# Performance work log

Hardware: AMD Instinct MI355X
Metric: run time of the kernel (lower is better)

Reference implementation:

```python
import jax, jax.numpy as jnp
import numpy as np

B, N, C = 16, 1024, 256
NH, DH = 8, 32          # dense attention heads
NHD, P = 8, 4           # deformable heads / sampling points
Hs = Ws = 32            # value spatial grid (N == Hs*Ws)
HID = 1024              # mlp hidden = 4*C


def setup_inputs() -> dict:
    key = jax.random.key(0)
    ks = jax.random.split(key, 16)
    rn = lambda i, shape, s=1.0: jax.random.normal(ks[i], shape, jnp.float32) * s
    return {
        "x": rn(0, (B, N, C)),
        "ref": jax.random.uniform(ks[1], (B, N, 2), jnp.float32),
        "value": rn(2, (B, N, C)),
        "ln1_w": jnp.ones((C,), jnp.float32), "ln1_b": jnp.zeros((C,), jnp.float32),
        "ln2_w": jnp.ones((C,), jnp.float32), "ln2_b": jnp.zeros((C,), jnp.float32),
        "ln3_w": jnp.ones((C,), jnp.float32), "ln3_b": jnp.zeros((C,), jnp.float32),
        "qkv_w": rn(3, (3 * C, C), 0.05),
        "proj_w": rn(4, (C, C), 0.05), "proj_b": jnp.zeros((C,), jnp.float32),
        "off_w": rn(5, (NHD * P * 2, C), 0.01), "off_b": rn(6, (NHD * P * 2,), 0.5),
        "aw_w": rn(7, (NHD * P, C), 0.01), "aw_b": jnp.zeros((NHD * P,), jnp.float32),
        "vproj_w": rn(8, (C, C), 0.05), "vproj_b": jnp.zeros((C,), jnp.float32),
        "oproj_w": rn(9, (C, C), 0.05), "oproj_b": jnp.zeros((C,), jnp.float32),
        "fc1_w": rn(10, (HID, C), 0.05), "fc1_b": jnp.zeros((HID,), jnp.float32),
        "fc2_w": rn(11, (C, HID), 0.05), "fc2_b": jnp.zeros((C,), jnp.float32),
    }


def _ln(x, w, b):
    m = x.mean(-1, keepdims=True)
    v = ((x - m) ** 2).mean(-1, keepdims=True)
    return (x - m) * jax.lax.rsqrt(v + 1e-5) * w + b


def _attn(x, qkv_w, proj_w, proj_b):
    qkv = (x @ qkv_w.T).reshape(B, N, 3, NH, DH)
    q, k, v = qkv[:, :, 0], qkv[:, :, 1], qkv[:, :, 2]
    a = jnp.einsum('bqhd,bkhd->bhqk', q, k) * (DH ** -0.5)
    a = jax.nn.softmax(a, axis=-1)
    o = jnp.einsum('bhqk,bkhd->bqhd', a, v).reshape(B, N, C)
    return o @ proj_w.T + proj_b


def _deform(q, ref, value, off_w, off_b, aw_w, aw_b, vproj_w, vproj_b, oproj_w, oproj_b):
    # single-level MS deformable attention (Deformable-DETR style)
    v = (value @ vproj_w.T + vproj_b).reshape(B, Hs * Ws, NHD, DH)
    off = (q @ off_w.T + off_b).reshape(B, N, NHD, P, 2)
    aw = jax.nn.softmax((q @ aw_w.T + aw_b).reshape(B, N, NHD, P), axis=-1)
    norm = jnp.array([Ws, Hs], jnp.float32)
    loc = ref[:, :, None, None, :] + off / norm  # [B,N,NHD,P,2] normalized coords
    gx = loc[..., 0] * Ws - 0.5
    gy = loc[..., 1] * Hs - 0.5
    x0 = jnp.floor(gx); y0 = jnp.floor(gy)
    lx = gx - x0; ly = gy - y0
    x0i = x0.astype(jnp.int32); y0i = y0.astype(jnp.int32)
    b_idx = jnp.arange(B)[:, None, None, None]
    h_idx = jnp.arange(NHD)[None, None, :, None]

    def gather(xi, yi):
        valid = ((xi >= 0) & (xi < Ws) & (yi >= 0) & (yi < Hs)).astype(jnp.float32)
        idx = jnp.clip(yi, 0, Hs - 1) * Ws + jnp.clip(xi, 0, Ws - 1)
        return v[b_idx, idx, h_idx] * valid[..., None]  # [B,N,NHD,P,DH]

    s = (gather(x0i, y0i) * ((1 - lx) * (1 - ly))[..., None]
         + gather(x0i + 1, y0i) * (lx * (1 - ly))[..., None]
         + gather(x0i, y0i + 1) * ((1 - lx) * ly)[..., None]
         + gather(x0i + 1, y0i + 1) * (lx * ly)[..., None])
    out = (s * aw[..., None]).sum(axis=3).reshape(B, N, C)
    return out @ oproj_w.T + oproj_b


def reference(x, ref, value, ln1_w, ln1_b, ln2_w, ln2_b, ln3_w, ln3_b,
              qkv_w, proj_w, proj_b, off_w, off_b, aw_w, aw_b,
              vproj_w, vproj_b, oproj_w, oproj_b, fc1_w, fc1_b, fc2_w, fc2_b):
    x = x + _attn(_ln(x, ln1_w, ln1_b), qkv_w, proj_w, proj_b)
    x = x + _deform(_ln(x, ln2_w, ln2_b), ref, value,
                    off_w, off_b, aw_w, aw_b, vproj_w, vproj_b, oproj_w, oproj_b)
    h = jax.nn.gelu(_ln(x, ln3_w, ln3_b) @ fc1_w.T + fc1_b, approximate=False) @ fc2_w.T + fc2_b
    return x + h
```

## Files before the change

kernel.cpp:

```cpp
#include <hip/hip_runtime.h>
#include <hip/hip_bf16.h>

#define Bq   16
#define Nq   1024
#define Cq   256
#define NHq  8
#define DHq  32
#define HIDq 1024
#define BNq  (Bq * Nq)

typedef float f32x4 __attribute__((ext_vector_type(4)));
typedef short bf16x8 __attribute__((ext_vector_type(8)));
typedef unsigned int u32x4 __attribute__((ext_vector_type(4)));
typedef unsigned short ushort_t;

__device__ __forceinline__ unsigned int f2bf(float f) {
    unsigned int u = __builtin_bit_cast(unsigned int, f);
    u = (u + 0x7fffu + ((u >> 16) & 1u)) >> 16;
    return u & 0xffffu;
}
__device__ __forceinline__ unsigned int packbf2(float a, float b) {
    unsigned int ua = __builtin_bit_cast(unsigned int, a) + 0x8000u;
    unsigned int ub = __builtin_bit_cast(unsigned int, b) + 0x8000u;
    return __builtin_amdgcn_perm(ub, ua, 0x07060302);
}
__device__ __forceinline__ unsigned int cvtpk_bf16(float lo, float hi) {
    unsigned int r;
    asm("v_cvt_pk_bf16_f32 %0, %1, %2" : "=v"(r) : "v"(lo), "v"(hi));
    return r;
}
__device__ __forceinline__ float gelu_t(float x) {
    float y = x * (0.7978845608028654f + 0.035677408136300125f * x * x);
    float e = __builtin_amdgcn_exp2f(y * 2.8853900817779268f);
    return x - x / (1.f + e);
}

typedef __attribute__((address_space(1))) const unsigned int* gas_u32;
typedef __attribute__((address_space(3))) unsigned int* las_u32;
__device__ __forceinline__ void gload16(const void* g, void* l) {
    __builtin_amdgcn_global_load_lds((gas_u32)g, (las_u32)l, 16, 0, 0);
}

struct CastSeg { const float* src; ushort_t* dst; int nblk; int n; };
struct CastArgs { CastSeg s[9]; };

__global__ __launch_bounds__(256) void castm(CastArgs a) {
    int bid = blockIdx.x;
    int seg = 0, acc = 0;
    for (seg = 0; seg < 9; seg++) {
        if (bid < acc + a.s[seg].nblk) break;
        acc += a.s[seg].nblk;
    }
    const CastSeg sg = a.s[seg];
    int i = (bid - acc) * 1024 + threadIdx.x * 4;
    if (i < sg.n) {
        float4 v = *(const float4*)(sg.src + i);
        uint2 u;
        u.x = packbf2(v.x, v.y);
        u.y = packbf2(v.z, v.w);
        *(uint2*)(sg.dst + i) = u;
    }
}

__global__ __launch_bounds__(256) void ln_kernel(const float* __restrict__ X,
                                                 const float* __restrict__ w,
                                                 const float* __restrict__ b,
                                                 ushort_t* __restrict__ Y) {
    int wave = threadIdx.x >> 6, lane = threadIdx.x & 63;
    int t = blockIdx.x * 4 + wave;
    float4 v = *(const float4*)(X + (size_t)t * Cq + lane * 4);
    float s = v.x + v.y + v.z + v.w;
#pragma unroll
    for (int d = 1; d < 64; d <<= 1) s += __shfl_xor(s, d);
    float mean = s * (1.f / 256.f);
    float4 dv = {v.x - mean, v.y - mean, v.z - mean, v.w - mean};
    float q = dv.x * dv.x + dv.y * dv.y + dv.z * dv.z + dv.w * dv.w;
#pragma unroll
    for (int d = 1; d < 64; d <<= 1) q += __shfl_xor(q, d);
    float rs = rsqrtf(q * (1.f / 256.f) + 1e-5f);
    float4 wv = *(const float4*)(w + lane * 4);
    float4 bv = *(const float4*)(b + lane * 4);
    uint2 u;
    u.x = packbf2(dv.x * rs * wv.x + bv.x, dv.y * rs * wv.y + bv.y);
    u.y = packbf2(dv.z * rs * wv.z + bv.z, dv.w * rs * wv.w + bv.w);
    *(uint2*)(Y + (size_t)t * Cq + lane * 4) = u;
}

template <int OMODE, bool GELU_, bool RESID, int KT>
__global__ __launch_bounds__(256) void mgemm(const ushort_t* __restrict__ A,
                                             const ushort_t* __restrict__ W,
                                             const float* __restrict__ bias,
                                             const float* __restrict__ R,
                                             void* __restrict__ OutP,
                                             int M, int Nn) {
    __shared__ __align__(16) ushort_t Al[2][8192];
    __shared__ __align__(16) ushort_t Bl[2][4096];
    int m0 = blockIdx.x * 128, n0 = blockIdx.y * 64;
    int tid = threadIdx.x;
    int w = tid >> 6, lane = tid & 63;
    int l15 = lane & 15, quad = lane >> 4;

    f32x4 acc[2][4];
#pragma unroll
    for (int i = 0; i < 2; i++)
#pragma unroll
        for (int j = 0; j < 4; j++) acc[i][j] = (f32x4){0.f, 0.f, 0.f, 0.f};

    const ushort_t* gA0 = A + (size_t)(m0 + lane) * KT + w * 8;
    const ushort_t* gA1 = gA0 + (size_t)64 * KT;
    const ushort_t* gB0 = W + (size_t)(n0 + lane) * KT + w * 8;

    auto STAGE = [&](int buf, int t) {
        const int k0 = t * 64;
        gload16(gA0 + k0,      &Al[buf][w * 1024]);
        gload16(gA1 + k0,      &Al[buf][w * 1024 + 512]);
        gload16(gA0 + k0 + 32, &Al[buf][(w + 4) * 1024]);
        gload16(gA1 + k0 + 32, &Al[buf][(w + 4) * 1024 + 512]);
        gload16(gB0 + k0,      &Bl[buf][w * 512]);
        gload16(gB0 + k0 + 32, &Bl[buf][(w + 4) * 512]);
    };

    constexpr int NT = KT / 64;
    STAGE(0, 0);
    STAGE(1, 1);
    asm volatile("s_waitcnt vmcnt(6)" ::: "memory");
    __builtin_amdgcn_s_barrier();

#pragma unroll
    for (int t = 0; t < NT; t++) {
        const int cur = t & 1;
        bf16x8 aF[2][2], bF[2][4];
#pragma unroll
        for (int ks = 0; ks < 2; ks++) {
#pragma unroll
            for (int i = 0; i < 2; i++)
                aF[ks][i] = *(const bf16x8*)&Al[cur][(ks * 4 + quad) * 1024 + (w * 32 + i * 16 + l15) * 8];
#pragma unroll
            for (int j = 0; j < 4; j++)
                bF[ks][j] = *(const bf16x8*)&Bl[cur][(ks * 4 + quad) * 512 + (j * 16 + l15) * 8];
        }
        asm volatile("s_waitcnt lgkmcnt(0)" ::: "memory");
        __builtin_amdgcn_sched_barrier(0);
        __builtin_amdgcn_s_barrier();
        if (t + 2 < NT) STAGE(cur, t + 2);

        __builtin_amdgcn_s_setprio(1);
#pragma unroll
        for (int ks = 0; ks < 2; ks++)
#pragma unroll
            for (int i = 0; i < 2; i++)
#pragma unroll
                for (int j = 0; j < 4; j++)
                    acc[i][j] = __builtin_amdgcn_mfma_f32_16x16x32_bf16(bF[ks][j], aF[ks][i], acc[i][j], 0, 0, 0);
        __builtin_amdgcn_s_setprio(0);

        if (t + 2 < NT) {
            asm volatile("s_waitcnt vmcnt(6)" ::: "memory");
        } else if (t + 1 < NT) {
            asm volatile("s_waitcnt vmcnt(0)" ::: "memory");
        }
        if (t + 1 < NT) __builtin_amdgcn_s_barrier();
    }

#pragma unroll
    for (int i = 0; i < 2; i++) {
        int mg = m0 + w * 32 + i * 16 + l15;
#pragma unroll
        for (int j = 0; j < 4; j++) {
            int ng = n0 + j * 16 + quad * 4;
            f32x4 rv = acc[i][j];
            if constexpr (OMODE == 1) {
                int which = ng >> 8;
                int h = (ng >> 5) & 7;
                int d = ng & 31;
                int bb = mg >> 10, nn = mg & 1023;
                ushort_t* qb = (ushort_t*)OutP;
                if (which == 2) {
                    size_t dst = 2 * (size_t)BNq * Cq +
                                 ((size_t)(bb * 8 + h) * 32 + d) * 1024 + nn;
#pragma unroll
                    for (int r = 0; r < 4; r++)
                        qb[dst + (size_t)r * 1024] = (ushort_t)f2bf(rv[r]);
                } else {
                    if (which == 0) {
                        const float sc = 0.17677669529663687f * 1.4426950408889634f;
                        rv[0] *= sc; rv[1] *= sc; rv[2] *= sc; rv[3] *= sc;
                    }
                    size_t dst = (size_t)which * ((size_t)BNq * Cq) +
                                 ((size_t)(bb * 8 + h) * 1024 + nn) * 32 + d;
                    uint2 pk;
                    pk.x = packbf2(rv[0], rv[1]);
                    pk.y = packbf2(rv[2], rv[3]);
                    *(uint2*)(qb + dst) = pk;
                }
            } else if constexpr (OMODE == 3) {
                if (ng >= 96) continue;
                if (ng < 64) {
                    float4 bv = *(const float4*)(bias + ng);
                    rv[0] += bv.x; rv[1] += bv.y; rv[2] += bv.z; rv[3] += bv.w;
                    *(float4*)((float*)OutP + (size_t)mg * 64 + ng) =
                        make_float4(rv[0], rv[1], rv[2], rv[3]);
                } else {
                    float4 bv = *(const float4*)(R + (ng - 64));
                    rv[0] += bv.x; rv[1] += bv.y; rv[2] += bv.z; rv[3] += bv.w;
                    *(float4*)((float*)OutP + (size_t)BNq * 64 + (size_t)mg * 32 + (ng - 64)) =
                        make_float4(rv[0], rv[1], rv[2], rv[3]);
                }
            } else {
                if (bias) {
                    float4 bv = *(const float4*)(bias + ng);
                    rv[0] += bv.x; rv[1] += bv.y; rv[2] += bv.z; rv[3] += bv.w;
                }
                if (GELU_) {
#pragma unroll
                    for (int r = 0; r < 4; r++) rv[r] = gelu_t(rv[r]);
                }
                if constexpr (OMODE == 2) {
                    uint2 pk;
                    pk.x = packbf2(rv[0], rv[1]);
                    pk.y = packbf2(rv[2], rv[3]);
                    *(uint2*)((ushort_t*)OutP + (size_t)mg * Nn + ng) = pk;
                } else {
                    if (RESID) {
                        float4 rr = *(const float4*)(R + (size_t)mg * Nn + ng);
                        rv[0] += rr.x; rv[1] += rr.y; rv[2] += rr.z; rv[3] += rr.w;
                    }
                    *(float4*)((float*)OutP + (size_t)mg * Nn + ng) =
                        make_float4(rv[0], rv[1], rv[2], rv[3]);
                }
            }
        }
    }
}

__global__ __launch_bounds__(256) void mlp_fused(const float* __restrict__ X,
                                                 const ushort_t* __restrict__ W1,
                                                 const float* __restrict__ b1,
                                                 const ushort_t* __restrict__ W2,
                                                 const float* __restrict__ b2,
                                                 const float* __restrict__ lnw,
                                                 const float* __restrict__ lnb,
                                                 float* __restrict__ out) {
    __shared__ __align__(16) ushort_t W1l[16384];
    __shared__ __align__(16) ushort_t W2l[8192];
    __shared__ __align__(16) ushort_t Hl[4096];
    __shared__ __align__(16) float b1l[1024];
    __shared__ __align__(16) float lnwl[256];
    __shared__ __align__(16) float lnbl[256];
    int bid = blockIdx.x;
    int m0 = (bid >> 1) * 64;
    int nh = bid & 1;
    int tid = threadIdx.x;
    int w = tid >> 6, lane = tid & 63;
    int l15 = lane & 15, quad = lane >> 4;

    auto SW1 = [&](int ch) {
        const ushort_t* g = W1 + (size_t)(ch * 64 + lane) * 256 + w * 8;
#pragma unroll
        for (int j = 0; j < 8; j++)
            gload16(g + j * 32, &W1l[(w + 4 * j) * 512]);
    };
    auto SW2 = [&](int ch) {
#pragma unroll
        for (int jj = 0; jj < 4; jj++) {
            const int kc2 = (jj & 1) * 4 + w;
            const int rj = jj >> 1;
            const ushort_t* g = W2 + (size_t)(nh * 128 + rj * 64 + lane) * 1024 +
                                ch * 64 + (kc2 & 3) * 8 + (kc2 >> 2) * 32;
            gload16(g, &W2l[kc2 * 1024 + rj * 512]);
        }
    };

    f32x4 acc2[4][2];
#pragma unroll
    for (int i = 0; i < 4; i++)
#pragma unroll
        for (int j = 0; j < 2; j++) acc2[i][j] = (f32x4){0.f, 0.f, 0.f, 0.f};

    SW1(0);
    SW2(0);
    gload16(b1 + w * 256 + lane * 4, &b1l[w * 256]);
    if (w == 0) gload16(lnw + lane * 4, &lnwl[0]);
    if (w == 1) gload16(lnb + lane * 4, &lnbl[0]);

    float4 xv[16];
    {
        const float* gx = X + (size_t)(m0 + w * 16 + l15) * 256 + quad * 8;
#pragma unroll
        for (int ks = 0; ks < 8; ks++) {
            xv[2 * ks]     = *(const float4*)(gx + ks * 32);
            xv[2 * ks + 1] = *(const float4*)(gx + ks * 32 + 4);
        }
    }
    asm volatile("s_waitcnt vmcnt(0)" ::: "memory");
    __builtin_amdgcn_s_barrier();

    float s = 0.f;
#pragma unroll
    for (int i = 0; i < 16; i++) s += xv[i].x + xv[i].y + xv[i].z + xv[i].w;
    s += __shfl_xor(s, 16);
    s += __shfl_xor(s, 32);
    float mean = s * (1.f / 256.f);
    float q = 0.f;
#pragma unroll
    for (int i = 0; i < 16; i++) {
        float a0 = xv[i].x - mean, a1 = xv[i].y - mean;
        float a2 = xv[i].z - mean, a3 = xv[i].w - mean;
        q += a0 * a0 + a1 * a1 + a2 * a2 + a3 * a3;
    }
    q += __shfl_xor(q, 16);
    q += __shfl_xor(q, 32);
    float rs = rsqrtf(q * (1.f / 256.f) + 1e-5f);

    bf16x8 aF[8];
#pragma unroll
    for (int ks = 0; ks < 8; ks++) {
        const int kb = ks * 32 + quad * 8;
        float y0 = (xv[2 * ks].x - mean) * rs * lnwl[kb + 0] + lnbl[kb + 0];
        float y1 = (xv[2 * ks].y - mean) * rs * lnwl[kb + 1] + lnbl[kb + 1];
        float y2 = (xv[2 * ks].z - mean) * rs * lnwl[kb + 2] + lnbl[kb + 2];
        float y3 = (xv[2 * ks].w - mean) * rs * lnwl[kb + 3] + lnbl[kb + 3];
        float y4 = (xv[2 * ks + 1].x - mean) * rs * lnwl[kb + 4] + lnbl[kb + 4];
        float y5 = (xv[2 * ks + 1].y - mean) * rs * lnwl[kb + 5] + lnbl[kb + 5];
        float y6 = (xv[2 * ks + 1].z - mean) * rs * lnwl[kb + 6] + lnbl[kb + 6];
        float y7 = (xv[2 * ks + 1].w - mean) * rs * lnwl[kb + 7] + lnbl[kb + 7];
        u32x4 up;
        up.x = cvtpk_bf16(y0, y1);
        up.y = cvtpk_bf16(y2, y3);
        up.z = cvtpk_bf16(y4, y5);
        up.w = cvtpk_bf16(y6, y7);
        aF[ks] = __builtin_bit_cast(bf16x8, up);
    }

    for (int ch = 0; ch < 16; ch++) {
        f32x4 acc1[4];
#pragma unroll
        for (int j = 0; j < 4; j++) acc1[j] = (f32x4){0.f, 0.f, 0.f, 0.f};
#pragma unroll
        for (int ks = 0; ks < 8; ks++) {
            bf16x8 bF[4];
#pragma unroll
            for (int j = 0; j < 4; j++)
                bF[j] = *(const bf16x8*)&W1l[(ks * 4 + quad) * 512 + (j * 16 + l15) * 8];
#pragma unroll
            for (int j = 0; j < 4; j++)
                acc1[j] = __builtin_amdgcn_mfma_f32_16x16x32_bf16(bF[j], aF[ks], acc1[j], 0, 0, 0);
        }
#pragma unroll
        for (int j = 0; j < 4; j++) {
            float4 b1v = *(const float4*)&b1l[ch * 64 + j * 16 + quad * 4];
            f32x4 rv = acc1[j];
            rv[0] = gelu_t(rv[0] + b1v.x);
            rv[1] = gelu_t(rv[1] + b1v.y);
            rv[2] = gelu_t(rv[2] + b1v.z);
            rv[3] = gelu_t(rv[3] + b1v.w);
            int h = j * 16 + quad * 4;
            uint2 pk;
            pk.x = cvtpk_bf16(rv[0], rv[1]);
            pk.y = cvtpk_bf16(rv[2], rv[3]);
            *(uint2*)&Hl[((h >> 3) * 64 + (w * 16 + l15)) * 8 + (h & 7)] = pk;
        }
        asm volatile("s_waitcnt lgkmcnt(0)" ::: "memory");
        __builtin_amdgcn_sched_barrier(0);
        __builtin_amdgcn_s_barrier();
        if (ch + 1 < 16) {
            SW1(ch + 1);
            asm volatile("s_waitcnt vmcnt(8)" ::: "memory");
        } else {
            asm volatile("s_waitcnt vmcnt(0)" ::: "memory");
        }
        __builtin_amdgcn_s_barrier();

        __builtin_amdgcn_s_setprio(1);
#pragma unroll
        for (int ks2 = 0; ks2 < 2; ks2++) {
            bf16x8 a2[4], b2f[2];
#pragma unroll
            for (int i = 0; i < 4; i++)
                a2[i] = *(const bf16x8*)&Hl[(ks2 * 4 + quad) * 512 + (i * 16 + l15) * 8];
#pragma unroll
            for (int j = 0; j < 2; j++)
                b2f[j] = *(const bf16x8*)&W2l[(ks2 * 4 + quad) * 1024 + (w * 32 + j * 16 + l15) * 8];
#pragma unroll
            for (int i = 0; i < 4; i++)
#pragma unroll
                for (int j = 0; j < 2; j++)
                    acc2[i][j] = __builtin_amdgcn_mfma_f32_16x16x32_bf16(b2f[j], a2[i], acc2[i][j], 0, 0, 0);
        }
        __builtin_amdgcn_s_setprio(0);
        asm volatile("s_waitcnt lgkmcnt(0)" ::: "memory");
        __builtin_amdgcn_sched_barrier(0);
        __builtin_amdgcn_s_barrier();
        if (ch + 1 < 16) {
            SW2(ch + 1);
            asm volatile("s_waitcnt vmcnt(4)" ::: "memory");
            __builtin_amdgcn_s_barrier();
        }
    }

#pragma unroll
    for (int i = 0; i < 4; i++) {
        int mg = m0 + i * 16 + l15;
#pragma unroll
        for (int j = 0; j < 2; j++) {
            int ng = nh * 128 + w * 32 + j * 16 + quad * 4;
            f32x4 rv = acc2[i][j];
            float4 bv = *(const float4*)(b2 + ng);
            float4 rr = *(const float4*)(X + (size_t)mg * 256 + ng);
            rv[0] += bv.x + rr.x; rv[1] += bv.y + rr.y;
            rv[2] += bv.z + rr.z; rv[3] += bv.w + rr.w;
            *(float4*)(out + (size_t)mg * 256 + ng) =
                make_float4(rv[0], rv[1], rv[2], rv[3]);
        }
    }
}

__global__ __launch_bounds__(256, 4) void attn_mfma(const ushort_t* __restrict__ Qb,
                                                    const ushort_t* __restrict__ Kb,
                                                    const ushort_t* __restrict__ Vtg,
                                                    ushort_t* __restrict__ o) {
    int bh = blockIdx.x;
    int b = bh >> 3, h = bh & 7;
    int q0 = blockIdx.y * 128;
    int tid = threadIdx.x;
    int wave = tid >> 6, lane = tid & 63;
    int l15 = lane & 15, quad = lane >> 4;

    __shared__ __align__(16) ushort_t Ks[2][64][40];
    __shared__ __align__(16) ushort_t Vs[2][32][88];
    __shared__ __align__(16) ushort_t Ps[4][32][72];

    const size_t hb = (size_t)bh * 32768;

    bf16x8 qfrag[2];
#pragma unroll
    for (int g = 0; g < 2; g++)
        qfrag[g] = *(const bf16x8*)(Qb + hb + (size_t)(q0 + wave * 32 + g * 16 + l15) * 32 + quad * 8);

    f32x4 oa[2][2];
#pragma unroll
    for (int g = 0; g < 2; g++)
#pragma unroll
        for (int t = 0; t < 2; t++) oa[g][t] = (f32x4){0.f, 0.f, 0.f, 0.f};
    f32x4 ls[2];
    ls[0] = (f32x4){0.f, 0.f, 0.f, 0.f};
    ls[1] = (f32x4){0.f, 0.f, 0.f, 0.f};

    bf16x8 ones;
#pragma unroll
    for (int i = 0; i < 8; i++) ones[i] = (short)0x3F80;

    int krow = tid >> 2, kch = tid & 3;
    int vrow = tid >> 3, vch = tid & 7;
    const ushort_t* kgp = Kb + hb + (size_t)krow * 32 + kch * 8;
    const ushort_t* vgp = Vtg + hb + (size_t)vrow * 1024 + vch * 8;

    bf16x8 kreg = *(const bf16x8*)kgp;
    bf16x8 vreg = *(const bf16x8*)vgp;

#pragma unroll 2
    for (int kt = 0; kt < 16; kt++) {
        const int cur = kt & 1;
        *(bf16x8*)&Ks[cur][krow][kch * 8] = kreg;
        *(bf16x8*)&Vs[cur][vrow][vch * 8] = vreg;
        __syncthreads();
        if (kt < 15) {
            kreg = *(const bf16x8*)(kgp + (kt + 1) * 2048);
            vreg = *(const bf16x8*)(vgp + (kt + 1) * 64);
        }

        bf16x8 kf[4];
#pragma unroll
        for (int kg = 0; kg < 4; kg++)
            kf[kg] = *(const bf16x8*)&Ks[cur][kg * 16 + l15][quad * 8];

        const f32x4 z = {0.f, 0.f, 0.f, 0.f};
#pragma unroll
        for (int g = 0; g < 2; g++) {
#pragma unroll
            for (int kg = 0; kg < 4; kg++) {
                f32x4 st = __builtin_amdgcn_mfma_f32_16x16x32_bf16(kf[kg], qfrag[g], z, 0, 0, 0);
                float e0 = __builtin_amdgcn_exp2f(st[0]);
                float e1 = __builtin_amdgcn_exp2f(st[1]);
                float e2 = __builtin_amdgcn_exp2f(st[2]);
                float e3 = __builtin_amdgcn_exp2f(st[3]);
                uint2 pk;
                pk.x = cvtpk_bf16(e0, e1);
                pk.y = cvtpk_bf16(e2, e3);
                *(uint2*)&Ps[wave][g * 16 + l15][kg * 16 + quad * 4] = pk;
            }
        }

        __builtin_amdgcn_s_setprio(1);
#pragma unroll
        for (int c = 0; c < 2; c++) {
            bf16x8 vb0 = *(const bf16x8*)&Vs[cur][l15][c * 32 + quad * 8];
            bf16x8 vb1 = *(const bf16x8*)&Vs[cur][16 + l15][c * 32 + quad * 8];
#pragma unroll
            for (int g = 0; g < 2; g++) {
                bf16x8 pa = *(const bf16x8*)&Ps[wave][g * 16 + l15][c * 32 + quad * 8];
                oa[g][0] = __builtin_amdgcn_mfma_f32_16x16x32_bf16(pa, vb0, oa[g][0], 0, 0, 0);
                oa[g][1] = __builtin_amdgcn_mfma_f32_16x16x32_bf16(pa, vb1, oa[g][1], 0, 0, 0);
                ls[g]    = __builtin_amdgcn_mfma_f32_16x16x32_bf16(pa, ones, ls[g], 0, 0, 0);
            }
        }
        __builtin_amdgcn_s_setprio(0);
    }

#pragma unroll
    for (int g = 0; g < 2; g++) {
#pragma unroll
        for (int r = 0; r < 4; r++) {
            float inv = 1.f / ls[g][r];
            int q = q0 + wave * 32 + g * 16 + quad * 4 + r;
            ushort_t* orow = o + ((size_t)(b * 1024 + q)) * 256 + h * 32;
            orow[l15] = (ushort_t)f2bf(oa[g][0][r] * inv);
            orow[l15 + 16] = (ushort_t)f2bf(oa[g][1][r] * inv);
        }
    }
}

__global__ __launch_bounds__(256) void deform_kernel(const float* __restrict__ ref,
                                                     const float* __restrict__ off,
                                                     const float* __restrict__ awl,
                                                     const float* __restrict__ v,
                                                     ushort_t* __restrict__ out) {
    int t = blockIdx.x;
    int b = t >> 10;
    int tid = threadIdx.x;
    int h = tid >> 5, d = tid & 31;

    float rx = ref[(size_t)t * 2 + 0];
    float ry = ref[(size_t)t * 2 + 1];
    const float* offr = off + (size_t)t * 64 + h * 8;
    const float* awr = awl + (size_t)t * 32 + h * 4;

    float L0 = awr[0], L1 = awr[1], L2 = awr[2], L3 = awr[3];
    float mm = fmaxf(fmaxf(L0, L1), fmaxf(L2, L3));
    float e0 = __expf(L0 - mm), e1 = __expf(L1 - mm), e2 = __expf(L2 - mm), e3 = __expf(L3 - mm);
    float inv = 1.f / (e0 + e1 + e2 + e3);
    float aw[4] = {e0 * inv, e1 * inv, e2 * inv, e3 * inv};

    const float* vb = v + (size_t)b * Nq * Cq + h * 32 + d;

    float s = 0.f;
#pragma unroll
    for (int p = 0; p < 4; p++) {
        float gx = rx * 32.f + offr[p * 2 + 0] - 0.5f;
        float gy = ry * 32.f + offr[p * 2 + 1] - 0.5f;
        float x0f = floorf(gx), y0f = floorf(gy);
        float lx = gx - x0f, ly = gy - y0f;
        int x0 = (int)x0f, y0 = (int)y0f;
        auto g = [&](int xi, int yi) -> float {
            if (xi < 0 || xi > 31 || yi < 0 || yi > 31) return 0.f;
            return vb[(size_t)(yi * 32 + xi) * Cq];
        };
        float sp = g(x0, y0) * (1.f - lx) * (1.f - ly)
                 + g(x0 + 1, y0) * lx * (1.f - ly)
                 + g(x0, y0 + 1) * (1.f - lx) * ly
                 + g(x0 + 1, y0 + 1) * lx * ly;
        s += aw[p] * sp;
    }
    out[(size_t)t * Cq + h * 32 + d] = (ushort_t)f2bf(s);
}

extern "C" void kernel_launch(void* const* d_in, const int* in_sizes, int n_in,
                              void* d_out, int out_size, void* d_ws, size_t ws_size,
                              hipStream_t stream) {
    const size_t S = (size_t)BNq * Cq;
    float* ws = (float*)d_ws;
    float* X = ws;
    ushort_t* Ybf = (ushort_t*)(ws + S);
    ushort_t* Wbf = (ushort_t*)(ws + S + S / 2);

    ushort_t* Wqkv   = Wbf;
    ushort_t* Wproj  = Wbf + 196608;
    ushort_t* Woff   = Wbf + 262144;
    ushort_t* Waw    = Wbf + 278528;
    ushort_t* Wvproj = Wbf + 286720;
    ushort_t* Woproj = Wbf + 352256;
    ushort_t* Wfc1   = Wbf + 417792;
    ushort_t* Wfc2   = Wbf + 679936;

    ushort_t* QKVbf = (ushort_t*)(ws + 2 * S);
    ushort_t* O1bf  = (ushort_t*)(ws + 2 * S + 3 * S / 2);
    float* Vb   = ws + 2 * S + S / 2;
    float* OffB = ws + 2 * S + 3 * S / 2;
    float* AwB  = OffB + (size_t)BNq * 64;
    ushort_t* Sbbf = (ushort_t*)(AwB + (size_t)BNq * 32);
    ushort_t* Valbf = (ushort_t*)(ws + 9 * S / 2);

    auto fp = [&](int i) { return (const float*)d_in[i]; };
    const float* x_in = fp(0);

    CastArgs ca;
    ca.s[0] = {fp(9),  Wqkv,   192, 196608};
    ca.s[1] = {fp(10), Wproj,  64,  65536};
    ca.s[2] = {fp(12), Woff,   16,  16384};
    ca.s[3] = {fp(14), Waw,    8,   8192};
    ca.s[4] = {fp(16), Wvproj, 64,  65536};
    ca.s[5] = {fp(18), Woproj, 64,  65536};
    ca.s[6] = {fp(20), Wfc1,   256, 262144};
    ca.s[7] = {fp(22), Wfc2,   256, 262144};
    ca.s[8] = {fp(2),  Valbf,  4096, (int)S};
    castm<<<5016, 256, 0, stream>>>(ca);

    ln_kernel<<<BNq / 4, 256, 0, stream>>>(x_in, fp(3), fp(4), Ybf);
    mgemm<1, false, false, 256><<<dim3(128, 12), 256, 0, stream>>>(
        Ybf, Wqkv, nullptr, nullptr, QKVbf, BNq, 768);
    attn_mfma<<<dim3(128, 8), 256, 0, stream>>>(
        QKVbf, QKVbf + S, QKVbf + 2 * S, O1bf);
    mgemm<0, false, true, 256><<<dim3(128, 4), 256, 0, stream>>>(
        O1bf, Wproj, fp(11), x_in, X, BNq, 256);

    ln_kernel<<<BNq / 4, 256, 0, stream>>>(X, fp(5), fp(6), Ybf);
    mgemm<0, false, false, 256><<<dim3(128, 4), 256, 0, stream>>>(
        Valbf, Wvproj, fp(17), nullptr, Vb, BNq, 256);
    mgemm<3, false, false, 256><<<dim3(128, 2), 256, 0, stream>>>(
        Ybf, Woff, fp(13), fp(15), OffB, BNq, 96);
    deform_kernel<<<BNq, 256, 0, stream>>>(fp(1), OffB, AwB, Vb, Sbbf);
    mgemm<0, false, true, 256><<<dim3(128, 4), 256, 0, stream>>>(
        Sbbf, Woproj, fp(19), X, X, BNq, 256);

    mlp_fused<<<BNq / 32, 256, 0, stream>>>(
        X, Wfc1, fp(21), Wfc2, fp(23), fp(7), fp(8), (float*)d_out);
}
```

Baseline: 315.8 us.

## Fuse LayerNorm into QKV and offset/attention-weight GEMMs via new lgemm kernel

Removes the standalone ln_kernel launches and adds an lgemm kernel. It loads fp32 rows, computes LayerNorm in registers, converts the result to bf16 A fragments and multiplies against double-buffered weight chunks in LDS. This avoids writing and re-reading the normalized bf16 activation buffer and drops two launches. In exchange it uses a different tiling (64-row tiles with register-resident A) and only 512 or 256 blocks, which may lower occupancy and parallelism compared with the previous mgemm grid.

```diff
diff --git a/kernel.cpp b/kernel.cpp
--- a/kernel.cpp
+++ b/kernel.cpp
@@ -60,30 +60,6 @@
         u.y = packbf2(v.z, v.w);
         *(uint2*)(sg.dst + i) = u;
     }
-}
-
-__global__ __launch_bounds__(256) void ln_kernel(const float* __restrict__ X,
-                                                 const float* __restrict__ w,
-                                                 const float* __restrict__ b,
-                                                 ushort_t* __restrict__ Y) {
-    int wave = threadIdx.x >> 6, lane = threadIdx.x & 63;
-    int t = blockIdx.x * 4 + wave;
-    float4 v = *(const float4*)(X + (size_t)t * Cq + lane * 4);
-    float s = v.x + v.y + v.z + v.w;
-#pragma unroll
-    for (int d = 1; d < 64; d <<= 1) s += __shfl_xor(s, d);
-    float mean = s * (1.f / 256.f);
-    float4 dv = {v.x - mean, v.y - mean, v.z - mean, v.w - mean};
-    float q = dv.x * dv.x + dv.y * dv.y + dv.z * dv.z + dv.w * dv.w;
-#pragma unroll
-    for (int d = 1; d < 64; d <<= 1) q += __shfl_xor(q, d);
-    float rs = rsqrtf(q * (1.f / 256.f) + 1e-5f);
-    float4 wv = *(const float4*)(w + lane * 4);
-    float4 bv = *(const float4*)(b + lane * 4);
-    uint2 u;
-    u.x = packbf2(dv.x * rs * wv.x + bv.x, dv.y * rs * wv.y + bv.y);
-    u.y = packbf2(dv.z * rs * wv.z + bv.z, dv.w * rs * wv.w + bv.w);
-    *(uint2*)(Y + (size_t)t * Cq + lane * 4) = u;
 }
 
 template <int OMODE, bool GELU_, bool RESID, int KT>
@@ -169,6 +145,134 @@
         for (int j = 0; j < 4; j++) {
             int ng = n0 + j * 16 + quad * 4;
             f32x4 rv = acc[i][j];
+            if (bias) {
+                float4 bv = *(const float4*)(bias + ng);
+                rv[0] += bv.x; rv[1] += bv.y; rv[2] += bv.z; rv[3] += bv.w;
+            }
+            if (GELU_) {
+#pragma unroll
+                for (int r = 0; r < 4; r++) rv[r] = gelu_t(rv[r]);
+            }
+            if constexpr (OMODE == 2) {
+                uint2 pk;
+                pk.x = packbf2(rv[0], rv[1]);
+                pk.y = packbf2(rv[2], rv[3]);
+                *(uint2*)((ushort_t*)OutP + (size_t)mg * Nn + ng) = pk;
+            } else {
+                if (RESID) {
+                    float4 rr = *(const float4*)(R + (size_t)mg * Nn + ng);
+                    rv[0] += rr.x; rv[1] += rr.y; rv[2] += rr.z; rv[3] += rr.w;
+                }
+                *(float4*)((float*)OutP + (size_t)mg * Nn + ng) =
+                    make_float4(rv[0], rv[1], rv[2], rv[3]);
+            }
+        }
+    }
+}
+
+template <int OMODE, int NCH, int NSPLIT>
+__global__ __launch_bounds__(256) void lgemm(const float* __restrict__ X,
+                                             const ushort_t* __restrict__ W,
+                                             const float* __restrict__ bias,
+                                             const float* __restrict__ R,
+                                             const float* __restrict__ lnw,
+                                             const float* __restrict__ lnb,
+                                             void* __restrict__ OutP) {
+    __shared__ __align__(16) ushort_t Wl[2][16384];
+    __shared__ __align__(16) float lnwl[256];
+    __shared__ __align__(16) float lnbl[256];
+    int bid = blockIdx.x;
+    int m0 = (bid / NSPLIT) * 64;
+    int nb = (bid % NSPLIT) * (NCH * 64);
+    int tid = threadIdx.x;
+    int w = tid >> 6, lane = tid & 63;
+    int l15 = lane & 15, quad = lane >> 4;
+
+    auto SW = [&](int buf, int ch) {
+        const ushort_t* g = W + (size_t)(nb + ch * 64 + lane) * 256 + w * 8;
+#pragma unroll
+        for (int j = 0; j < 8; j++)
+            gload16(g + j * 32, &Wl[buf][(w + 4 * j) * 512]);
+    };
+
+    SW(0, 0);
+    if (w == 0) gload16(lnw + lane * 4, &lnwl[0]);
+    if (w == 1) gload16(lnb + lane * 4, &lnbl[0]);
+    float4 xv[16];
+    {
+        const float* gx = X + (size_t)(m0 + w * 16 + l15) * 256 + quad * 8;
+#pragma unroll
+        for (int ks = 0; ks < 8; ks++) {
+            xv[2 * ks]     = *(const float4*)(gx + ks * 32);
+            xv[2 * ks + 1] = *(const float4*)(gx + ks * 32 + 4);
+        }
+    }
+    if (NCH > 1) SW(1, 1);
+    if (NCH > 1) { asm volatile("s_waitcnt vmcnt(8)" ::: "memory"); }
+    else         { asm volatile("s_waitcnt vmcnt(0)" ::: "memory"); }
+    __builtin_amdgcn_s_barrier();
+
+    float s = 0.f;
+#pragma unroll
+    for (int i = 0; i < 16; i++) s += xv[i].x + xv[i].y + xv[i].z + xv[i].w;
+    s += __shfl_xor(s, 16);
+    s += __shfl_xor(s, 32);
+    float mean = s * (1.f / 256.f);
+    float q = 0.f;
+#pragma unroll
+    for (int i = 0; i < 16; i++) {
+        float a0 = xv[i].x - mean, a1 = xv[i].y - mean;
+        float a2 = xv[i].z - mean, a3 = xv[i].w - mean;
+        q += a0 * a0 + a1 * a1 + a2 * a2 + a3 * a3;
+    }
+    q += __shfl_xor(q, 16);
+    q += __shfl_xor(q, 32);
+    float rs = rsqrtf(q * (1.f / 256.f) + 1e-5f);
+
+    bf16x8 aF[8];
+#pragma unroll
+    for (int ks = 0; ks < 8; ks++) {
+        const int kb = ks * 32 + quad * 8;
+        float y0 = (xv[2 * ks].x - mean) * rs * lnwl[kb + 0] + lnbl[kb + 0];
+        float y1 = (xv[2 * ks].y - mean) * rs * lnwl[kb + 1] + lnbl[kb + 1];
+        float y2 = (xv[2 * ks].z - mean) * rs * lnwl[kb + 2] + lnbl[kb + 2];
+        float y3 = (xv[2 * ks].w - mean) * rs * lnwl[kb + 3] + lnbl[kb + 3];
+        float y4 = (xv[2 * ks + 1].x - mean) * rs * lnwl[kb + 4] + lnbl[kb + 4];
+        float y5 = (xv[2 * ks + 1].y - mean) * rs * lnwl[kb + 5] + lnbl[kb + 5];
+        float y6 = (xv[2 * ks + 1].z - mean) * rs * lnwl[kb + 6] + lnbl[kb + 6];
+        float y7 = (xv[2 * ks + 1].w - mean) * rs * lnwl[kb + 7] + lnbl[kb + 7];
+        u32x4 up;
+        up.x = cvtpk_bf16(y0, y1);
+        up.y = cvtpk_bf16(y2, y3);
+        up.z = cvtpk_bf16(y4, y5);
+        up.w = cvtpk_bf16(y6, y7);
+        aF[ks] = __builtin_bit_cast(bf16x8, up);
+    }
+
+#pragma unroll
+    for (int ch = 0; ch < NCH; ch++) {
+        const int cur = ch & 1;
+        f32x4 acc[4];
+#pragma unroll
+        for (int j = 0; j < 4; j++) acc[j] = (f32x4){0.f, 0.f, 0.f, 0.f};
+        __builtin_amdgcn_s_setprio(1);
+#pragma unroll
+        for (int ks = 0; ks < 8; ks++) {
+            bf16x8 bF[4];
+#pragma unroll
+            for (int j = 0; j < 4; j++)
+                bF[j] = *(const bf16x8*)&Wl[cur][(ks * 4 + quad) * 512 + (j * 16 + l15) * 8];
+#pragma unroll
+            for (int j = 0; j < 4; j++)
+                acc[j] = __builtin_amdgcn_mfma_f32_16x16x32_bf16(bF[j], aF[ks], acc[j], 0, 0, 0);
+        }
+        __builtin_amdgcn_s_setprio(0);
+
+        int mg = m0 + w * 16 + l15;
+#pragma unroll
+        for (int j = 0; j < 4; j++) {
+            int ng = nb + ch * 64 + j * 16 + quad * 4;
+            f32x4 rv = acc[j];
             if constexpr (OMODE == 1) {
                 int which = ng >> 8;
                 int h = (ng >> 5) & 7;
@@ -193,7 +297,7 @@
                     pk.y = packbf2(rv[2], rv[3]);
                     *(uint2*)(qb + dst) = pk;
                 }
-            } else if constexpr (OMODE == 3) {
+            } else {
                 if (ng >= 96) continue;
                 if (ng < 64) {
                     float4 bv = *(const float4*)(bias + ng);
@@ -206,30 +310,19 @@
                     *(float4*)((float*)OutP + (size_t)BNq * 64 + (size_t)mg * 32 + (ng - 64)) =
                         make_float4(rv[0], rv[1], rv[2], rv[3]);
                 }
-            } else {
-                if (bias) {
-                    float4 bv = *(const float4*)(bias + ng);
-                    rv[0] += bv.x; rv[1] += bv.y; rv[2] += bv.z; rv[3] += bv.w;
-                }
-                if (GELU_) {
-#pragma unroll
-                    for (int r = 0; r < 4; r++) rv[r] = gelu_t(rv[r]);
-                }
-                if constexpr (OMODE == 2) {
-                    uint2 pk;
-                    pk.x = packbf2(rv[0], rv[1]);
-                    pk.y = packbf2(rv[2], rv[3]);
-                    *(uint2*)((ushort_t*)OutP + (size_t)mg * Nn + ng) = pk;
-                } else {
-                    if (RESID) {
-                        float4 rr = *(const float4*)(R + (size_t)mg * Nn + ng);
-                        rv[0] += rr.x; rv[1] += rr.y; rv[2] += rr.z; rv[3] += rr.w;
-                    }
-                    *(float4*)((float*)OutP + (size_t)mg * Nn + ng) =
-                        make_float4(rv[0], rv[1], rv[2], rv[3]);
-                }
             }
         }
+
+        asm volatile("s_waitcnt lgkmcnt(0)" ::: "memory");
+        __builtin_amdgcn_sched_barrier(0);
+        __builtin_amdgcn_s_barrier();
+        if (ch + 2 < NCH) {
+            SW(cur, ch + 2);
+            asm volatile("s_waitcnt vmcnt(8)" ::: "memory");
+        } else if (ch + 1 < NCH) {
+            asm volatile("s_waitcnt vmcnt(0)" ::: "memory");
+        }
+        if (ch + 1 < NCH) __builtin_amdgcn_s_barrier();
     }
 }
 
@@ -570,7 +663,6 @@
     const size_t S = (size_t)BNq * Cq;
     float* ws = (float*)d_ws;
     float* X = ws;
-    ushort_t* Ybf = (ushort_t*)(ws + S);
     ushort_t* Wbf = (ushort_t*)(ws + S + S / 2);
 
     ushort_t* Wqkv   = Wbf;
@@ -605,19 +697,17 @@
     ca.s[8] = {fp(2),  Valbf,  4096, (int)S};
     castm<<<5016, 256, 0, stream>>>(ca);
 
-    ln_kernel<<<BNq / 4, 256, 0, stream>>>(x_in, fp(3), fp(4), Ybf);
-    mgemm<1, false, false, 256><<<dim3(128, 12), 256, 0, stream>>>(
-        Ybf, Wqkv, nullptr, nullptr, QKVbf, BNq, 768);
+    lgemm<1, 6, 2><<<512, 256, 0, stream>>>(
+        x_in, Wqkv, nullptr, nullptr, fp(3), fp(4), QKVbf);
     attn_mfma<<<dim3(128, 8), 256, 0, stream>>>(
         QKVbf, QKVbf + S, QKVbf + 2 * S, O1bf);
     mgemm<0, false, true, 256><<<dim3(128, 4), 256, 0, stream>>>(
         O1bf, Wproj, fp(11), x_in, X, BNq, 256);
 
-    ln_kernel<<<BNq / 4, 256, 0, stream>>>(X, fp(5), fp(6), Ybf);
     mgemm<0, false, false, 256><<<dim3(128, 4), 256, 0, stream>>>(
         Valbf, Wvproj, fp(17), nullptr, Vb, BNq, 256);
-    mgemm<3, false, false, 256><<<dim3(128, 2), 256, 0, stream>>>(
-        Ybf, Woff, fp(13), fp(15), OffB, BNq, 96);
+    lgemm<3, 2, 1><<<256, 256, 0, stream>>>(
+        X, Woff, fp(13), fp(15), fp(5), fp(6), OffB);
     deform_kernel<<<BNq, 256, 0, stream>>>(fp(1), OffB, AwB, Vb, Sbbf);
     mgemm<0, false, true, 256><<<dim3(128, 4), 256, 0, stream>>>(
         Sbbf, Woproj, fp(19), X, X, BNq, 256);
```

Result: faster. 302.7 us (-4.1%).
